# Optimization experiments

Measured on AMD Instinct MI355X. Metric: run time of the kernel, lower is better.

Reference implementation:

```python
import jax, jax.numpy as jnp
import numpy as np

B, S, HIDDEN = 2, 2048, 2048
NUM_HEADS, NUM_KV_HEADS, HEAD_DIM = 16, 4, 128
Q_SIZE = NUM_HEADS * HEAD_DIM          # 2048
KV_SIZE = NUM_KV_HEADS * HEAD_DIM      # 512
ROPE_THETA = 10000.0
NEG = -1e30


def setup_inputs() -> dict:
    key = jax.random.key(0)
    k1, k2, k3 = jax.random.split(key, 3)
    hidden_states = jax.random.normal(k1, (B, S, HIDDEN), jnp.float32)
    w_qkv = jax.random.normal(k2, (HIDDEN, Q_SIZE + 2 * KV_SIZE), jnp.float32) / np.sqrt(HIDDEN)
    w_o = jax.random.normal(k3, (Q_SIZE, HIDDEN), jnp.float32) / np.sqrt(Q_SIZE)
    positions = jnp.broadcast_to(jnp.arange(S, dtype=jnp.int32), (B, S))
    return {"positions": positions, "hidden_states": hidden_states,
            "w_qkv": w_qkv, "w_o": w_o}


def _rope(x, positions):
    # x: [B, S, H, D], neox-style rotate-half rope over full head_dim
    d = x.shape[-1]
    inv_freq = 1.0 / (ROPE_THETA ** (jnp.arange(0, d, 2, dtype=jnp.float32) / d))
    ang = positions[..., None].astype(jnp.float32) * inv_freq      # [B, S, D/2]
    cos = jnp.cos(ang)[:, :, None, :]
    sin = jnp.sin(ang)[:, :, None, :]
    x1, x2 = jnp.split(x, 2, axis=-1)
    return jnp.concatenate([x1 * cos - x2 * sin, x2 * cos + x1 * sin], axis=-1)


def reference(positions, hidden_states, w_qkv, w_o):
    qkv = jnp.einsum('bsh,ho->bso', hidden_states, w_qkv)
    q, k, v = jnp.split(qkv, [Q_SIZE, Q_SIZE + KV_SIZE], axis=-1)
    q = q.reshape(B, S, NUM_HEADS, HEAD_DIM)
    k = k.reshape(B, S, NUM_KV_HEADS, HEAD_DIM)
    v = v.reshape(B, S, NUM_KV_HEADS, HEAD_DIM)
    q = _rope(q, positions)
    k = _rope(k, positions)
    rep = NUM_HEADS // NUM_KV_HEADS
    k = jnp.repeat(k, rep, axis=2)   # GQA expand -> [B, S, NUM_HEADS, D]
    v = jnp.repeat(v, rep, axis=2)
    scale = HEAD_DIM ** -0.5
    scores = jnp.einsum('bqhd,bkhd->bhqk', q, k) * scale   # [B, H, S, S]
    causal = jnp.tril(jnp.ones((S, S), dtype=bool))
    scores = jnp.where(causal, scores, NEG)
    probs = jax.nn.softmax(scores, axis=-1)
    attn = jnp.einsum('bhqk,bkhd->bqhd', probs, v).reshape(B, S, Q_SIZE)
    return jnp.einsum('bsq,qh->bsh', attn, w_o)
```

## Files before the change

kernel.cpp:

```cpp
#include <hip/hip_runtime.h>
#include <hip/hip_bf16.h>
#include <stdint.h>

#define BDIM 2
#define SDIM 2048
#define HID 2048
#define NH 16
#define NKV 4
#define HD 128
#define QSZ 2048
#define KVSZ 512
#define QKVW 3072
#define TOK (BDIM*SDIM)

typedef __attribute__((ext_vector_type(8))) short bf16x8;
typedef __attribute__((ext_vector_type(4))) float f32x4;
typedef __attribute__((ext_vector_type(16))) float f32x16;

__device__ __forceinline__ short f2bf(float f) {
  return (short)__bfloat16_as_ushort(__float2bfloat16(f));
}

__device__ __forceinline__ float exp2_fast(float x) {
  float r;
  asm("v_exp_f32 %0, %1" : "=v"(r) : "v"(x));
  return r;
}

__device__ __forceinline__ void gload_lds16(const void* g, void* lds) {
  __builtin_amdgcn_global_load_lds(
      (const __attribute__((address_space(1))) void*)g,
      (__attribute__((address_space(3))) void*)lds, 16, 0, 0);
}

__global__ __launch_bounds__(256) void k_cvt_bf16(const float* __restrict__ in,
                                                  short* __restrict__ out, int n) {
  int i = (blockIdx.x * 256 + threadIdx.x) * 4;
  if (i >= n) return;
  float4 v = *(const float4*)(in + i);
  short4 o; o.x = f2bf(v.x); o.y = f2bf(v.y); o.z = f2bf(v.z); o.w = f2bf(v.w);
  *(short4*)(out + i) = o;
}

__global__ __launch_bounds__(256) void k_transpose_cvt(const float* __restrict__ in,
                                                       short* __restrict__ out,
                                                       int R, int C) {
  __shared__ short tile[64][65];
  int k0 = blockIdx.y * 64;
  int n0 = blockIdx.x * 64;
  int t = threadIdx.x;
#pragma unroll
  for (int i = 0; i < 16; ++i) {
    int idx = i * 256 + t;
    int kk = idx >> 6, nn = idx & 63;
    tile[kk][nn] = f2bf(in[(size_t)(k0 + kk) * C + n0 + nn]);
  }
  __syncthreads();
#pragma unroll
  for (int i = 0; i < 16; ++i) {
    int idx = i * 256 + t;
    int nn = idx >> 6, kk = idx & 63;
    out[(size_t)(n0 + nn) * R + k0 + kk] = tile[kk][nn];
  }
}

__global__ __launch_bounds__(256) void k_gemm_bf16(const short* __restrict__ A,
                                                   const short* __restrict__ Bt,
                                                   float* __restrict__ C,
                                                   int M, int N, int K) {
  __shared__ char lds[128 * 32 * 2 * 2];
  char* As = lds;
  char* Bs = lds + 8192;
  const int tid = threadIdx.x;
  const int w = tid >> 6, l = tid & 63;
  const int lq = l & 15, g = l >> 4;
  const int m0 = blockIdx.y * 128, n0 = blockIdx.x * 128;
  const int wm = (w >> 1) * 64, wn = (w & 1) * 64;
  f32x4 acc[4][4] = {};

  const int nk = K >> 5;
  for (int kt = 0; kt < nk; ++kt) {
    const int k0 = kt * 32;
#pragma unroll
    for (int i = 0; i < 2; ++i) {
      int ch = (w + 4 * i) * 64 + l;
      int r = ch >> 2, cc = ch & 3;
      int gc = cc ^ ((r >> 1) & 3);
      gload_lds16(A + (size_t)(m0 + r) * K + k0 + gc * 8, As + (w + 4 * i) * 1024);
      gload_lds16(Bt + (size_t)(n0 + r) * K + k0 + gc * 8, Bs + (w + 4 * i) * 1024);
    }
    __syncthreads();
    bf16x8 af[4], bfr[4];
#pragma unroll
    for (int mi = 0; mi < 4; ++mi) {
      int row = wm + mi * 16 + lq;
      af[mi] = *(const bf16x8*)(As + row * 64 + ((g ^ ((row >> 1) & 3)) * 16));
    }
#pragma unroll
    for (int ni = 0; ni < 4; ++ni) {
      int row = wn + ni * 16 + lq;
      bfr[ni] = *(const bf16x8*)(Bs + row * 64 + ((g ^ ((row >> 1) & 3)) * 16));
    }
#pragma unroll
    for (int mi = 0; mi < 4; ++mi)
#pragma unroll
      for (int ni = 0; ni < 4; ++ni)
        acc[mi][ni] = __builtin_amdgcn_mfma_f32_16x16x32_bf16(af[mi], bfr[ni],
                                                              acc[mi][ni], 0, 0, 0);
    __syncthreads();
  }
#pragma unroll
  for (int mi = 0; mi < 4; ++mi)
#pragma unroll
    for (int ni = 0; ni < 4; ++ni)
#pragma unroll
      for (int r = 0; r < 4; ++r) {
        int row = m0 + wm + mi * 16 + 4 * g + r;
        int col = n0 + wn + ni * 16 + lq;
        C[(size_t)row * N + col] = acc[mi][ni][r];
      }
}

__global__ __launch_bounds__(256) void k_gemm_qkv_rope(const short* __restrict__ A,
                                                       const short* __restrict__ Bt,
                                                       const int* __restrict__ pos,
                                                       short* __restrict__ Qh,
                                                       short* __restrict__ Kh,
                                                       short* __restrict__ VT) {
  __shared__ char lds[128 * 32 * 2 * 2];
  char* As = lds;
  char* Bs = lds + 8192;
  const int tid = threadIdx.x;
  const int w = tid >> 6, l = tid & 63;
  const int lq = l & 15, g = l >> 4;
  const int m0 = blockIdx.y * 128, n0 = blockIdx.x * 128;
  const int K = HID, N = QKVW;
  f32x4 acc[2][8] = {};

  const int nk = K >> 5;
  for (int kt = 0; kt < nk; ++kt) {
    const int k0 = kt * 32;
#pragma unroll
    for (int i = 0; i < 2; ++i) {
      int ch = (w + 4 * i) * 64 + l;
      int r = ch >> 2, cc = ch & 3;
      int gc = cc ^ ((r >> 1) & 3);
      gload_lds16(A + (size_t)(m0 + r) * K + k0 + gc * 8, As + (w + 4 * i) * 1024);
      gload_lds16(Bt + (size_t)(n0 + r) * K + k0 + gc * 8, Bs + (w + 4 * i) * 1024);
    }
    __syncthreads();
    bf16x8 af[2], bfr[8];
#pragma unroll
    for (int mi = 0; mi < 2; ++mi) {
      int row = w * 32 + mi * 16 + lq;
      af[mi] = *(const bf16x8*)(As + row * 64 + ((g ^ ((row >> 1) & 3)) * 16));
    }
#pragma unroll
    for (int ni = 0; ni < 8; ++ni) {
      int row = ni * 16 + lq;
      bfr[ni] = *(const bf16x8*)(Bs + row * 64 + ((g ^ ((row >> 1) & 3)) * 16));
    }
#pragma unroll
    for (int mi = 0; mi < 2; ++mi)
#pragma unroll
      for (int ni = 0; ni < 8; ++ni)
        acc[mi][ni] = __builtin_amdgcn_mfma_f32_16x16x32_bf16(af[mi], bfr[ni],
                                                              acc[mi][ni], 0, 0, 0);
    __syncthreads();
  }

  const int hx = blockIdx.x;
  const int b = m0 >> 11;
  if (hx < 20) {
    const float qscale = 0.12751743920f;
    const float sc = (hx < 16) ? qscale : 1.0f;
    short* dst = (hx < 16) ? (Qh + (size_t)(b * NH + hx) * SDIM * HD)
                           : (Kh + (size_t)(b * NKV + (hx - 16)) * SDIM * HD);
    float invf[4];
#pragma unroll
    for (int ni = 0; ni < 4; ++ni)
      invf[ni] = expf(-(float)(ni * 16 + lq) * (9.210340371976184f / 64.0f));
#pragma unroll
    for (int mi = 0; mi < 2; ++mi)
#pragma unroll
      for (int r = 0; r < 4; ++r) {
        int row = m0 + w * 32 + mi * 16 + 4 * g + r;
        int s = row & (SDIM - 1);
        float p = (float)pos[row];
        size_t hb = (size_t)s * HD;
#pragma unroll
        for (int ni = 0; ni < 4; ++ni) {
          float sn, cs;
          sincosf(p * invf[ni], &sn, &cs);
          float x1 = acc[mi][ni][r], x2 = acc[mi][ni + 4][r];
          dst[hb + ni * 16 + lq] = f2bf((x1 * cs - x2 * sn) * sc);
          dst[hb + ni * 16 + lq + 64] = f2bf((x2 * cs + x1 * sn) * sc);
        }
      }
  } else {
    const int hv = hx - 20;
    const int s00 = (m0 & (SDIM - 1)) + w * 32;
#pragma unroll
    for (int mi = 0; mi < 2; ++mi)
#pragma unroll
      for (int ni = 0; ni < 8; ++ni) {
        int d = ni * 16 + lq;
        int s0 = s00 + mi * 16 + 4 * g;
        size_t vb = ((size_t)(b * NKV + hv) * HD + d) * SDIM + s0;
        short4 ov;
        ov.x = f2bf(acc[mi][ni][0]); ov.y = f2bf(acc[mi][ni][1]);
        ov.z = f2bf(acc[mi][ni][2]); ov.w = f2bf(acc[mi][ni][3]);
        *(short4*)(VT + vb) = ov;
      }
  }
}

__global__ __launch_bounds__(256, 3) void k_attn(const short* __restrict__ Qh,
                                                 const short* __restrict__ Kh,
                                                 const short* __restrict__ VT,
                                                 short* __restrict__ attn, int S) {
  __shared__ char lds[2][16384];
  const int tid = threadIdx.x;
  const int w = tid >> 6, l = tid & 63;
  const int l31 = l & 31, hi = l >> 5;
  const int nqc = S / 128;
  const int bid = blockIdx.x;
  const int b = bid / (NH * nqc);
  const int rem = bid % (NH * nqc);
  const int h = rem / nqc;
  const int qc = nqc - 1 - (rem % nqc);
  const int q0 = qc * 128 + w * 32;
  const int kvh = h >> 2;
  const short* Qp = Qh + (size_t)(b * NH + h) * S * HD;
  const short* Kp = Kh + (size_t)(b * NKV + kvh) * S * HD;
  const short* Vp = VT + (size_t)(b * NKV + kvh) * HD * S;

  bf16x8 qf[8];
#pragma unroll
  for (int kc = 0; kc < 8; ++kc)
    qf[kc] = *(const bf16x8*)(Qp + (size_t)(q0 + l31) * HD + kc * 16 + hi * 8);

  f32x16 o[4] = {};
  float mrun = -1e30f, lrun = 0.f;
  const int qabs = q0 + l31;
  const int ntu = qc * 4 + 4;

#define STAGE(bufi, c0_)                                                          \
  {                                                                               \
    char* Kb = lds[bufi];                                                         \
    char* Vb = lds[bufi] + 8192;                                                  \
    _Pragma("unroll")                                                             \
    for (int i = 0; i < 2; ++i) {                                                 \
      int id = (i * 4 + w) * 64 + l;                                              \
      int kr = id >> 4, c16 = id & 15;                                            \
      gload_lds16(Kp + (size_t)((c0_) + kr) * HD + ((c16 ^ (kr & 7)) * 8),        \
                  Kb + (i * 4 + w) * 1024);                                       \
      int vr = id >> 2, c4 = id & 3;                                              \
      gload_lds16(Vp + (size_t)vr * S + (c0_) + ((c4 ^ ((vr >> 1) & 3)) * 8),     \
                  Vb + (i * 4 + w) * 1024);                                       \
    }                                                                             \
  }

  STAGE(0, 0);
  asm volatile("s_waitcnt vmcnt(0)" ::: "memory");
  __builtin_amdgcn_s_barrier();

  for (int c = 0; c < ntu; ++c) {
    const int c0 = c * 32;
    const int cur = c & 1;
    if (c + 1 < ntu) STAGE(cur ^ 1, c0 + 32);
    const char* Ks = lds[cur];
    const char* Vs = lds[cur] + 8192;

    f32x16 st = {};
    __builtin_amdgcn_s_setprio(1);
#pragma unroll
    for (int kc = 0; kc < 8; ++kc) {
      bf16x8 kf = *(const bf16x8*)(Ks + l31 * 256 + (((kc * 2 + hi) ^ (l31 & 7)) * 16));
      st = __builtin_amdgcn_mfma_f32_32x32x16_bf16(kf, qf[kc], st, 0, 0, 0);
    }
    __builtin_amdgcn_s_setprio(0);
    float tmax = -1e30f;
#pragma unroll
    for (int r = 0; r < 16; ++r) {
      int kv = c0 + (r & 3) + 8 * (r >> 2) + 4 * hi;
      float sv = (kv <= qabs) ? st[r] : -1e30f;
      st[r] = sv;
      tmax = fmaxf(tmax, sv);
    }
    tmax = fmaxf(tmax, __shfl_xor(tmax, 32));
    if (!__all(tmax - mrun <= 8.0f)) {
      float mnew = fmaxf(mrun, tmax);
      float fac = exp2_fast(mrun - mnew);
      lrun *= fac;
#pragma unroll
      for (int d0 = 0; d0 < 4; ++d0) o[d0] = o[d0] * fac;
      mrun = mnew;
    }
    float sum = 0.f;
#pragma unroll
    for (int r = 0; r < 16; ++r) {
      float e = exp2_fast(st[r] - mrun);
      st[r] = e;
      sum += e;
    }
    sum += __shfl_xor(sum, 32);
    lrun += sum;
    __builtin_amdgcn_s_setprio(1);
#pragma unroll
    for (int j = 0; j < 2; ++j) {
      uint32_t W0 = (uint32_t)(uint16_t)f2bf(st[8 * j + 0]) |
                    ((uint32_t)(uint16_t)f2bf(st[8 * j + 1]) << 16);
      uint32_t W1 = (uint32_t)(uint16_t)f2bf(st[8 * j + 2]) |
                    ((uint32_t)(uint16_t)f2bf(st[8 * j + 3]) << 16);
      uint32_t W2 = (uint32_t)(uint16_t)f2bf(st[8 * j + 4]) |
                    ((uint32_t)(uint16_t)f2bf(st[8 * j + 5]) << 16);
      uint32_t W3 = (uint32_t)(uint16_t)f2bf(st[8 * j + 6]) |
                    ((uint32_t)(uint16_t)f2bf(st[8 * j + 7]) << 16);
      uint32_t Y0 = __shfl_xor(hi ? W0 : W2, 32);
      uint32_t Y1 = __shfl_xor(hi ? W1 : W3, 32);
      union { uint32_t u[4]; bf16x8 v; } pu;
      pu.u[0] = hi ? Y0 : W0;
      pu.u[1] = hi ? Y1 : W1;
      pu.u[2] = hi ? W2 : Y0;
      pu.u[3] = hi ? W3 : Y1;
#pragma unroll
      for (int d0 = 0; d0 < 4; ++d0) {
        int vr = d0 * 32 + l31;
        bf16x8 vf = *(const bf16x8*)(Vs + vr * 64 + (((j * 2 + hi) ^ ((vr >> 1) & 3)) * 16));
        o[d0] = __builtin_amdgcn_mfma_f32_32x32x16_bf16(vf, pu.v, o[d0], 0, 0, 0);
      }
    }
    __builtin_amdgcn_s_setprio(0);
    asm volatile("s_waitcnt vmcnt(0)" ::: "memory");
    __builtin_amdgcn_s_barrier();
  }
#undef STAGE
  float inv = 1.0f / lrun;
  size_t rowb = (size_t)(b * S + q0 + l31) * QSZ + h * HD;
#pragma unroll
  for (int d0 = 0; d0 < 4; ++d0)
#pragma unroll
    for (int gq = 0; gq < 4; ++gq) {
      short4 ov;
      ov.x = f2bf(o[d0][4 * gq + 0] * inv);
      ov.y = f2bf(o[d0][4 * gq + 1] * inv);
      ov.z = f2bf(o[d0][4 * gq + 2] * inv);
      ov.w = f2bf(o[d0][4 * gq + 3] * inv);
      *(short4*)(attn + rowb + d0 * 32 + 8 * gq + 4 * hi) = ov;
    }
}

extern "C" void kernel_launch(void* const* d_in, const int* in_sizes, int n_in,
                              void* d_out, int out_size, void* d_ws, size_t ws_size,
                              hipStream_t stream) {
  const int* positions = (const int*)d_in[0];
  const float* hidden = (const float*)d_in[1];
  const float* w_qkv = (const float*)d_in[2];
  const float* w_o = (const float*)d_in[3];
  float* out = (float*)d_out;

  char* ws = (char*)d_ws;
  short* X     = (short*)(ws);
  short* WqkvT = (short*)(ws + 16777216);
  short* WoT   = (short*)(ws + 29360128);
  short* Qh    = (short*)(ws + 88080384);
  short* Kh    = (short*)(ws + 104857600);
  short* VT    = (short*)(ws + 109051904);
  short* ATT   = (short*)(ws + 113246208);

  k_cvt_bf16<<<8192, 256, 0, stream>>>(hidden, X, TOK * HID);
  k_transpose_cvt<<<dim3(QKVW / 64, HID / 64), 256, 0, stream>>>(w_qkv, WqkvT, HID, QKVW);
  k_transpose_cvt<<<dim3(HID / 64, QSZ / 64), 256, 0, stream>>>(w_o, WoT, QSZ, HID);
  k_gemm_qkv_rope<<<dim3(QKVW / 128, TOK / 128), 256, 0, stream>>>(X, WqkvT, positions,
                                                                   Qh, Kh, VT);
  k_attn<<<BDIM * NH * (SDIM / 128), 256, 0, stream>>>(Qh, Kh, VT, ATT, SDIM);
  k_gemm_bf16<<<dim3(HID / 128, TOK / 128), 256, 0, stream>>>(ATT, WoT, out, TOK, HID, QSZ);
}
```

Baseline: 238.6 us.

## Give each attention wave private KV buffers, drop barriers, trim causal work

The attention kernel now gives each wave its own LDS slot for K/V tiles. Each wave stages its own tiles, loads fragments into registers, then prefetches the next tile into the same buffer, so no block barriers are needed. Each wave loops only up to its own diagonal (q0/32+1 tiles instead of the block's), and the causal mask is applied only on the last tile. This costs 4x the LDS per block, 4x redundant global K/V loads within a block, and lower occupancy (launch bounds 3 to 2). RoPE sincos is also switched to hardware v_sin/v_cos on revolutions with exp2-based inverse frequencies, trading some accuracy for fewer instructions.

```diff
diff --git a/kernel.cpp b/kernel.cpp
--- a/kernel.cpp
+++ b/kernel.cpp
@@ -25,6 +25,14 @@
   float r;
   asm("v_exp_f32 %0, %1" : "=v"(r) : "v"(x));
   return r;
+}
+
+__device__ __forceinline__ void sincos_rev(float rev, float* sn, float* cs) {
+  float fr, s, c;
+  asm("v_fract_f32 %0, %1" : "=v"(fr) : "v"(rev));
+  asm("v_sin_f32 %0, %1" : "=v"(s) : "v"(fr));
+  asm("v_cos_f32 %0, %1" : "=v"(c) : "v"(fr));
+  *sn = s; *cs = c;
 }
 
 __device__ __forceinline__ void gload_lds16(const void* g, void* lds) {
@@ -134,7 +142,7 @@
   const int w = tid >> 6, l = tid & 63;
   const int lq = l & 15, g = l >> 4;
   const int m0 = blockIdx.y * 128, n0 = blockIdx.x * 128;
-  const int K = HID, N = QKVW;
+  const int K = HID;
   f32x4 acc[2][8] = {};
 
   const int nk = K >> 5;
@@ -179,7 +187,8 @@
     float invf[4];
 #pragma unroll
     for (int ni = 0; ni < 4; ++ni)
-      invf[ni] = expf(-(float)(ni * 16 + lq) * (9.210340371976184f / 64.0f));
+      invf[ni] = 0.15915494309f *
+                 exp2_fast(-(float)(ni * 16 + lq) * (13.287712379549449f / 64.0f));
 #pragma unroll
     for (int mi = 0; mi < 2; ++mi)
 #pragma unroll
@@ -191,7 +200,7 @@
 #pragma unroll
         for (int ni = 0; ni < 4; ++ni) {
           float sn, cs;
-          sincosf(p * invf[ni], &sn, &cs);
+          sincos_rev(p * invf[ni], &sn, &cs);
           float x1 = acc[mi][ni][r], x2 = acc[mi][ni + 4][r];
           dst[hb + ni * 16 + lq] = f2bf((x1 * cs - x2 * sn) * sc);
           dst[hb + ni * 16 + lq + 64] = f2bf((x2 * cs + x1 * sn) * sc);
@@ -215,11 +224,11 @@
   }
 }
 
-__global__ __launch_bounds__(256, 3) void k_attn(const short* __restrict__ Qh,
+__global__ __launch_bounds__(256, 2) void k_attn(const short* __restrict__ Qh,
                                                  const short* __restrict__ Kh,
                                                  const short* __restrict__ VT,
                                                  short* __restrict__ attn, int S) {
-  __shared__ char lds[2][16384];
+  __shared__ char lds[4][16384];
   const int tid = threadIdx.x;
   const int w = tid >> 6, l = tid & 63;
   const int l31 = l & 31, hi = l >> 5;
@@ -234,6 +243,8 @@
   const short* Qp = Qh + (size_t)(b * NH + h) * S * HD;
   const short* Kp = Kh + (size_t)(b * NKV + kvh) * S * HD;
   const short* Vp = VT + (size_t)(b * NKV + kvh) * HD * S;
+  char* Kb = lds[w];
+  char* Vb = lds[w] + 8192;
 
   bf16x8 qf[8];
 #pragma unroll
@@ -243,50 +254,63 @@
   f32x16 o[4] = {};
   float mrun = -1e30f, lrun = 0.f;
   const int qabs = q0 + l31;
-  const int ntu = qc * 4 + 4;
-
-#define STAGE(bufi, c0_)                                                          \
+  const int ntw = q0 / 32 + 1;
+
+#define STAGEKV(c0_)                                                              \
   {                                                                               \
-    char* Kb = lds[bufi];                                                         \
-    char* Vb = lds[bufi] + 8192;                                                  \
     _Pragma("unroll")                                                             \
-    for (int i = 0; i < 2; ++i) {                                                 \
-      int id = (i * 4 + w) * 64 + l;                                              \
+    for (int i = 0; i < 8; ++i) {                                                 \
+      int id = i * 64 + l;                                                        \
       int kr = id >> 4, c16 = id & 15;                                            \
-      gload_lds16(Kp + (size_t)((c0_) + kr) * HD + ((c16 ^ (kr & 7)) * 8),        \
-                  Kb + (i * 4 + w) * 1024);                                       \
+      gload_lds16(Kp + (size_t)((c0_) + kr) * HD + ((c16 ^ (kr & 15)) * 8),       \
+                  Kb + i * 1024);                                                 \
+    }                                                                             \
+    _Pragma("unroll")                                                             \
+    for (int i = 0; i < 8; ++i) {                                                 \
+      int id = i * 64 + l;                                                        \
       int vr = id >> 2, c4 = id & 3;                                              \
       gload_lds16(Vp + (size_t)vr * S + (c0_) + ((c4 ^ ((vr >> 1) & 3)) * 8),     \
-                  Vb + (i * 4 + w) * 1024);                                       \
+                  Vb + i * 1024);                                                 \
     }                                                                             \
   }
 
-  STAGE(0, 0);
+  STAGEKV(0);
   asm volatile("s_waitcnt vmcnt(0)" ::: "memory");
-  __builtin_amdgcn_s_barrier();
-
-  for (int c = 0; c < ntu; ++c) {
-    const int c0 = c * 32;
-    const int cur = c & 1;
-    if (c + 1 < ntu) STAGE(cur ^ 1, c0 + 32);
-    const char* Ks = lds[cur];
-    const char* Vs = lds[cur] + 8192;
-
+
+  for (int t = 0; t < ntw; ++t) {
+    const int c0 = t * 32;
+    bf16x8 kf[8], vf[8];
+#pragma unroll
+    for (int kc = 0; kc < 8; ++kc)
+      kf[kc] = *(const bf16x8*)(Kb + l31 * 256 + (((kc * 2 + hi) ^ (l31 & 15)) * 16));
+#pragma unroll
+    for (int j = 0; j < 2; ++j)
+#pragma unroll
+      for (int d0 = 0; d0 < 4; ++d0) {
+        int vr = d0 * 32 + l31;
+        vf[j * 4 + d0] =
+            *(const bf16x8*)(Vb + vr * 64 + (((j * 2 + hi) ^ ((vr >> 1) & 3)) * 16));
+      }
+    asm volatile("s_waitcnt lgkmcnt(0)" ::: "memory");
+    if (t + 1 < ntw) STAGEKV(c0 + 32);
     f32x16 st = {};
     __builtin_amdgcn_s_setprio(1);
 #pragma unroll
-    for (int kc = 0; kc < 8; ++kc) {
-      bf16x8 kf = *(const bf16x8*)(Ks + l31 * 256 + (((kc * 2 + hi) ^ (l31 & 7)) * 16));
-      st = __builtin_amdgcn_mfma_f32_32x32x16_bf16(kf, qf[kc], st, 0, 0, 0);
-    }
+    for (int kc = 0; kc < 8; ++kc)
+      st = __builtin_amdgcn_mfma_f32_32x32x16_bf16(kf[kc], qf[kc], st, 0, 0, 0);
     __builtin_amdgcn_s_setprio(0);
     float tmax = -1e30f;
-#pragma unroll
-    for (int r = 0; r < 16; ++r) {
-      int kv = c0 + (r & 3) + 8 * (r >> 2) + 4 * hi;
-      float sv = (kv <= qabs) ? st[r] : -1e30f;
-      st[r] = sv;
-      tmax = fmaxf(tmax, sv);
+    if (t + 1 < ntw) {
+#pragma unroll
+      for (int r = 0; r < 16; ++r) tmax = fmaxf(tmax, st[r]);
+    } else {
+#pragma unroll
+      for (int r = 0; r < 16; ++r) {
+        int kv = c0 + (r & 3) + 8 * (r >> 2) + 4 * hi;
+        float sv = (kv <= qabs) ? st[r] : -1e30f;
+        st[r] = sv;
+        tmax = fmaxf(tmax, sv);
+      }
     }
     tmax = fmaxf(tmax, __shfl_xor(tmax, 32));
     if (!__all(tmax - mrun <= 8.0f)) {
@@ -325,17 +349,14 @@
       pu.u[2] = hi ? W2 : Y0;
       pu.u[3] = hi ? W3 : Y1;
 #pragma unroll
-      for (int d0 = 0; d0 < 4; ++d0) {
-        int vr = d0 * 32 + l31;
-        bf16x8 vf = *(const bf16x8*)(Vs + vr * 64 + (((j * 2 + hi) ^ ((vr >> 1) & 3)) * 16));
-        o[d0] = __builtin_amdgcn_mfma_f32_32x32x16_bf16(vf, pu.v, o[d0], 0, 0, 0);
-      }
+      for (int d0 = 0; d0 < 4; ++d0)
+        o[d0] = __builtin_amdgcn_mfma_f32_32x32x16_bf16(vf[j * 4 + d0], pu.v,
+                                                        o[d0], 0, 0, 0);
     }
     __builtin_amdgcn_s_setprio(0);
     asm volatile("s_waitcnt vmcnt(0)" ::: "memory");
-    __builtin_amdgcn_s_barrier();
-  }
-#undef STAGE
+  }
+#undef STAGEKV
   float inv = 1.0f / lrun;
   size_t rowb = (size_t)(b * S + q0 + l31) * QSZ + h * HD;
 #pragma unroll
```

Result: slower. 256.4 us (+7.5%).
